# Optimization experiments

Measured on AMD Instinct MI355X. Metric: run time of the kernel, lower is better.

Reference implementation:

```python
import jax, jax.numpy as jnp
import numpy as np

B, S, D_MODEL = 2, 2048, 512
N_HEADS, D_KV = 8, 64
NUM_BUCKETS, MAX_DISTANCE = 32, 128


def _relative_position_bucket(relative_position, num_buckets=NUM_BUCKETS, max_distance=MAX_DISTANCE):
    # bidirectional (is_decoder=False) bucketing, exactly as HF T5
    num_buckets = num_buckets // 2
    buckets = (relative_position > 0).astype(jnp.int32) * num_buckets
    rel = jnp.abs(relative_position)
    max_exact = num_buckets // 2
    is_small = rel < max_exact
    rel_f = jnp.maximum(rel, 1).astype(jnp.float32)
    val_if_large = max_exact + (
        jnp.log(rel_f / max_exact) / np.log(max_distance / max_exact) * (num_buckets - max_exact)
    ).astype(jnp.int32)
    val_if_large = jnp.minimum(val_if_large, num_buckets - 1)
    return buckets + jnp.where(is_small, rel, val_if_large)


def _compute_bias(rel_bias_emb, q_len, k_len):
    ctx = jnp.arange(q_len)[:, None]          # [q,1]
    mem = jnp.arange(k_len)[None, :]          # [1,k]
    buckets = _relative_position_bucket(mem - ctx)        # [q,k] int32
    bias = rel_bias_emb[buckets]                           # [q,k,H]
    return jnp.transpose(bias, (2, 0, 1))[None]            # [1,H,q,k]


def setup_inputs() -> dict:
    key = jax.random.key(0)
    ks = jax.random.split(key, 6)
    sc = 1.0 / np.sqrt(D_MODEL)
    return {
        "hidden_states": jax.random.normal(ks[0], (B, S, D_MODEL), jnp.float32),
        "Wq": jax.random.normal(ks[1], (D_MODEL, N_HEADS * D_KV), jnp.float32) * sc,
        "Wk": jax.random.normal(ks[2], (D_MODEL, N_HEADS * D_KV), jnp.float32) * sc,
        "Wv": jax.random.normal(ks[3], (D_MODEL, N_HEADS * D_KV), jnp.float32) * sc,
        "Wo": jax.random.normal(ks[4], (N_HEADS * D_KV, D_MODEL), jnp.float32) * sc,
        "rel_bias_emb": jax.random.normal(ks[5], (NUM_BUCKETS, N_HEADS), jnp.float32),
    }


def reference(hidden_states, Wq, Wk, Wv, Wo, rel_bias_emb):
    b, s, _ = hidden_states.shape

    def proj(W):  # [b,s,D] @ [D,H*Dk] -> [b,H,s,Dk]
        return (hidden_states @ W).reshape(b, s, N_HEADS, D_KV).transpose(0, 2, 1, 3)

    q = proj(Wq)
    k = proj(Wk)
    v = proj(Wv)

    # T5 attention: NO 1/sqrt(d) scaling
    scores = jnp.einsum("bhqd,bhkd->bhqk", q, k)
    position_bias = _compute_bias(rel_bias_emb, s, s)      # [1,H,s,s]
    scores = scores + position_bias
    attn = jax.nn.softmax(scores.astype(jnp.float32), axis=-1).astype(scores.dtype)
    # dropout p=0.0 in eval mode -> identity
    out = jnp.einsum("bhqk,bhkd->bhqd", attn, v)           # [b,H,s,Dk]
    out = out.transpose(0, 2, 1, 3).reshape(b, s, N_HEADS * D_KV)
    attn_output = out @ Wo                                  # [b,s,D]
    return attn_output, position_bias
```

## Files before the change

kernel.cpp:

```cpp
#include <hip/hip_runtime.h>

typedef __attribute__((ext_vector_type(8))) short short8;
typedef __attribute__((ext_vector_type(4))) float f32x4;
typedef __attribute__((ext_vector_type(16))) float f32x16;
typedef __attribute__((ext_vector_type(4))) float float4v;
typedef __attribute__((ext_vector_type(8))) float f32x8;
typedef __attribute__((ext_vector_type(4))) unsigned short us4;
typedef __attribute__((ext_vector_type(8))) unsigned short us8v;
typedef __attribute__((ext_vector_type(4))) unsigned int uint4v;

#define DEVI __device__ __forceinline__
#define MFMA16(a,b,c) __builtin_amdgcn_mfma_f32_16x16x32_bf16((a),(b),(c),0,0,0)
#define MFMA32(a,b,c) __builtin_amdgcn_mfma_f32_32x32x16_bf16((a),(b),(c),0,0,0)

DEVI unsigned short f2bf(float x) {
    unsigned u = __builtin_bit_cast(unsigned, x);
    u += 0x7FFFu + ((u >> 16) & 1u);
    return (unsigned short)(u >> 16);
}
DEVI float bf2f(unsigned short b) {
    return __builtin_bit_cast(float, ((unsigned)b) << 16);
}
DEVI unsigned cvt_pk_bf16(float lo, float hi) {
    unsigned r;
    asm("v_cvt_pk_bf16_f32 %0, %1, %2" : "=v"(r) : "v"(lo), "v"(hi));
    return r;
}

__global__ __launch_bounds__(256) void k_prep_hidden(const float* __restrict__ hid,
                                                     unsigned short* __restrict__ hh,
                                                     unsigned short* __restrict__ hl) {
    __shared__ float tile[64][65];
    const int bid = blockIdx.x;
    const int rt = bid >> 3, ct = bid & 7;
    const int t = threadIdx.x;
    const int r = t >> 2, cc = (t & 3) << 4;
    const float* sp = hid + (long)(rt * 64 + r) * 512 + ct * 64 + cc;
    #pragma unroll
    for (int j = 0; j < 16; j += 4) {
        float4v v = *reinterpret_cast<const float4v*>(sp + j);
        tile[r][cc + j + 0] = v[0];
        tile[r][cc + j + 1] = v[1];
        tile[r][cc + j + 2] = v[2];
        tile[r][cc + j + 3] = v[3];
    }
    __syncthreads();
    #pragma unroll
    for (int s = 0; s < 2; ++s) {
        int slot = t * 2 + s;
        int lane = slot & 63, i = (slot >> 6) & 3, ktl = slot >> 8;
        int ri = i * 16 + (lane & 15);
        int kc = ktl * 32 + (lane >> 4) * 8;
        us8v hv, lv;
        #pragma unroll
        for (int j = 0; j < 8; ++j) {
            float x = tile[ri][kc + j];
            unsigned short hb = f2bf(x);
            hv[j] = hb; lv[j] = f2bf(x - bf2f(hb));
        }
        long o = ((long)(rt * 16 + ct * 2 + ktl) * 4 + i) * 512 + lane * 8;
        *reinterpret_cast<us8v*>(hh + o) = hv;
        *reinterpret_cast<us8v*>(hl + o) = lv;
    }
}

__global__ __launch_bounds__(256) void k_prep_w(const float* __restrict__ wq, const float* __restrict__ wk,
                                                const float* __restrict__ wvp, const float* __restrict__ wo,
                                                unsigned short* __restrict__ wqthi, unsigned short* __restrict__ wqtlo,
                                                unsigned short* __restrict__ wkthi, unsigned short* __restrict__ wktlo,
                                                unsigned short* __restrict__ wvt, unsigned short* __restrict__ wot) {
    __shared__ float tile[64][65];
    const int bid = blockIdx.x;
    const int mat = bid >> 6, t6 = bid & 63;
    const int tr = t6 >> 3, tc = t6 & 7;
    const float* src = mat == 0 ? wq : mat == 1 ? wk : mat == 2 ? wvp : wo;
    const int t = threadIdx.x;
    const int r = t >> 2, cc = (t & 3) << 4;
    const float* sp = src + (long)(tr * 64 + r) * 512 + tc * 64 + cc;
    #pragma unroll
    for (int j = 0; j < 16; j += 4) {
        float4v v = *reinterpret_cast<const float4v*>(sp + j);
        tile[r][cc + j + 0] = v[0];
        tile[r][cc + j + 1] = v[1];
        tile[r][cc + j + 2] = v[2];
        tile[r][cc + j + 3] = v[3];
    }
    __syncthreads();
    us8v h0, h1, l0, l1;
    #pragma unroll
    for (int j = 0; j < 8; ++j) {
        float x = tile[cc + j][r];
        unsigned short hb = f2bf(x);
        h0[j] = hb; l0[j] = f2bf(x - bf2f(hb));
        float y = tile[cc + 8 + j][r];
        unsigned short hb2 = f2bf(y);
        h1[j] = hb2; l1[j] = f2bf(y - bf2f(hb2));
    }
    if (mat <= 2) {
        const int jj = r >> 4, li = r & 15;
        const int kt = (tr * 64 + cc) >> 5;
        const int g0 = (cc >> 3) & 3;
        const long bse = ((long)((tc * 16 + kt) * 4 + jj)) * 512;
        const long o0 = bse + (g0 * 16 + li) * 8;
        const long o1 = bse + ((g0 + 1) * 16 + li) * 8;
        if (mat <= 1) {
            unsigned short* oh = mat ? wkthi : wqthi;
            unsigned short* ol = mat ? wktlo : wqtlo;
            *reinterpret_cast<us8v*>(oh + o0) = h0;
            *reinterpret_cast<us8v*>(oh + o1) = h1;
            *reinterpret_cast<us8v*>(ol + o0) = l0;
            *reinterpret_cast<us8v*>(ol + o1) = l1;
        } else {
            *reinterpret_cast<us8v*>(wvt + o0) = h0;
            *reinterpret_cast<us8v*>(wvt + o1) = h1;
        }
    } else {
        const long obase = (long)(tc * 64 + r) * 512 + tr * 64 + cc;
        *reinterpret_cast<us8v*>(wot + obase) = h0;
        *reinterpret_cast<us8v*>(wot + obase + 8) = h1;
    }
}

DEVI int bucket_large(int a) {
    if (a < 12) return 8;
    if (a < 16) return 9;
    if (a < 23) return 10;
    if (a < 32) return 11;
    if (a < 46) return 12;
    if (a < 64) return 13;
    if (a < 91) return 14;
    return 15;
}
__global__ __launch_bounds__(256) void k_prep_bias(const float* __restrict__ emb, float* __restrict__ biasT) {
    int t = blockIdx.x * 256 + threadIdx.x;
    if (t >= 8 * 4095) return;
    int h = t / 4095;
    int idx = t - h * 4095;
    int rel = idx - 2047;
    int a = rel < 0 ? -rel : rel;
    int bucket = (rel > 0 ? 16 : 0) + (a < 8 ? a : bucket_large(a));
    biasT[h * 4096 + idx] = emb[bucket * 8 + h];
}

__global__ __launch_bounds__(256) void k_proj(const unsigned short* __restrict__ hh,
                                              const unsigned short* __restrict__ hl,
                                              const unsigned short* __restrict__ wqthi, const unsigned short* __restrict__ wqtlo,
                                              const unsigned short* __restrict__ wkthi, const unsigned short* __restrict__ wktlo,
                                              const unsigned short* __restrict__ wvt,
                                              unsigned short* __restrict__ q_hi, unsigned short* __restrict__ q_lo,
                                              unsigned short* __restrict__ ktiles,
                                              unsigned short* __restrict__ vtiles) {
    const int wgid = blockIdx.x;
    const int nt = wgid % 12, mt = wgid / 12;
    const int sec = nt >> 2;
    const bool isv = (sec == 2);
    const int tid = threadIdx.x, wv = tid >> 6, lane = tid & 63;
    const int wr = wv >> 1, wc = wv & 1;
    const int g = lane >> 4, li = lane & 15;
    const int m0 = mt * 128 + wr * 64;
    const int n0 = (nt & 3) * 128 + wc * 64;
    const unsigned short* bh_ = (sec == 0) ? wqthi : (sec == 1) ? wkthi : wvt;
    const unsigned short* bl_ = (sec == 0) ? wqtlo : wktlo;
    const int rt2 = m0 >> 6;
    const int ntile = n0 >> 6;

    f32x4 zf = {0.f, 0.f, 0.f, 0.f};
    f32x4 acc[4][4];
    #pragma unroll
    for (int i = 0; i < 4; ++i)
        #pragma unroll
        for (int j = 0; j < 4; ++j) acc[i][j] = zf;

    for (int ks = 0; ks < 512; ks += 32) {
        const int kt = ks >> 5;
        const long abase = ((long)(rt2 * 16 + kt) * 4) * 512 + lane * 8;
        const long bbase = ((long)(ntile * 16 + kt) * 4) * 512 + lane * 8;
        short8 ah[4], al[4], bhf[4], blf[4];
        #pragma unroll
        for (int i = 0; i < 4; ++i) {
            ah[i] = *reinterpret_cast<const short8*>(hh + abase + i * 512);
            if (!isv) al[i] = *reinterpret_cast<const short8*>(hl + abase + i * 512);
            bhf[i] = *reinterpret_cast<const short8*>(bh_ + bbase + i * 512);
            if (!isv) blf[i] = *reinterpret_cast<const short8*>(bl_ + bbase + i * 512);
        }
        #pragma unroll
        for (int i = 0; i < 4; ++i)
            #pragma unroll
            for (int j = 0; j < 4; ++j) {
                acc[i][j] = MFMA16(ah[i], bhf[j], acc[i][j]);
                if (!isv) {
                    acc[i][j] = MFMA16(ah[i], blf[j], acc[i][j]);
                    acc[i][j] = MFMA16(al[i], bhf[j], acc[i][j]);
                }
            }
    }

    if (sec == 0) {
        #pragma unroll
        for (int i = 0; i < 4; ++i) {
            int rowb = m0 + i * 16 + g * 4;
            #pragma unroll
            for (int j = 0; j < 4; ++j) {
                int col = n0 + j * 16 + li;
                #pragma unroll
                for (int r = 0; r < 4; ++r) {
                    float x = acc[i][j][r];
                    unsigned short hb = f2bf(x);
                    long o = (long)(rowb + r) * 512 + col;
                    q_hi[o] = hb;
                    q_lo[o] = f2bf(x - bf2f(hb));
                }
            }
        }
    } else if (sec == 1) {
        #pragma unroll
        for (int i = 0; i < 4; ++i) {
            int rowb = m0 + i * 16 + g * 4;
            #pragma unroll
            for (int j = 0; j < 4; ++j) {
                int col = n0 + j * 16 + li;
                int h2 = col >> 6, d = col & 63;
                int ds2 = d >> 4, j2 = d & 7, lhalf = (d >> 3) & 1;
                #pragma unroll
                for (int r = 0; r < 4; ++r) {
                    int srow = rowb + r;
                    int bloc = srow >> 11, k = srow & 2047;
                    long base = (long)((bloc * 8 + h2) * 64 + (k >> 5)) * 4096
                              + (((k & 31) | (lhalf << 5)) * 8 + j2);
                    float x = acc[i][j][r];
                    unsigned short hb = f2bf(x);
                    ktiles[base + ds2 * 512] = hb;
                    ktiles[base + (4 + ds2) * 512] = f2bf(x - bf2f(hb));
                }
            }
        }
    } else {
        #pragma unroll
        for (int i = 0; i < 4; ++i) {
            int rowb = m0 + i * 16 + g * 4;
            int bloc = rowb >> 11, k = rowb & 2047;
            int kt = k >> 5, t = (k >> 4) & 1, lhalf = (k >> 3) & 1, j0 = k & 7;
            #pragma unroll
            for (int j = 0; j < 4; ++j) {
                int col = n0 + j * 16 + li;
                int h2 = col >> 6, d = col & 63;
                int dblk = d >> 5;
                us4 w;
                #pragma unroll
                for (int r = 0; r < 4; ++r) w[r] = f2bf(acc[i][j][r]);
                long off2 = (long)((bloc * 8 + h2) * 64 + kt) * 2048
                          + (dblk * 2 + t) * 512 + (((d & 31) | (lhalf << 5)) * 8 + j0);
                *reinterpret_cast<us4*>(vtiles + off2) = w;
            }
        }
    }
}

__global__ __launch_bounds__(128) void k_attn(const unsigned short* __restrict__ qhi,
                                              const unsigned short* __restrict__ qlo,
                                              const unsigned short* __restrict__ ktiles,
                                              const unsigned short* __restrict__ vtiles,
                                              const float* __restrict__ biasT,
                                              unsigned short* __restrict__ ctx) {
    __shared__ float lb[2080];
    __shared__ float mrg[64][34];
    const int wg = blockIdx.x;
    const int bh = wg >> 6, qt = wg & 63;
    const int b = bh >> 3, h = bh & 7;
    const int tid = threadIdx.x;
    const int kh = tid >> 6, lane = tid & 63;
    const int ql_ = lane & 31, hi = lane >> 5;
    const int q0 = qt * 32;

    for (int i = tid; i < 2080; i += 128) lb[i] = biasT[h * 4096 + (2016 - q0) + i];
    __syncthreads();

    const int q = q0 + ql_;
    const long rowQ = (long)(b * 2048 + q) * 512 + h * 64 + hi * 8;
    short8 qfh[4], qfl[4];
    #pragma unroll
    for (int ds = 0; ds < 4; ++ds) {
        qfh[ds] = *reinterpret_cast<const short8*>(qhi + rowQ + ds * 16);
        qfl[ds] = *reinterpret_cast<const short8*>(qlo + rowQ + ds * 16);
    }
    const int kbeg = kh * 1024;
    const unsigned short* ktb = ktiles + ((long)bh * 64 + (kbeg >> 5)) * 4096;
    const unsigned short* vtb = vtiles + ((long)bh * 64 + (kbeg >> 5)) * 2048;

    f32x16 o0, o1;
    #pragma unroll
    for (int i = 0; i < 16; ++i) { o0[i] = 0.f; o1[i] = 0.f; }
    float m_run = -__builtin_inff(), l_run = 0.f;

    short8 kAh[4], kAl[4], kBh[4], kBl[4], vA[4], vB[4];
    #pragma unroll
    for (int ds = 0; ds < 4; ++ds) {
        kAh[ds] = *reinterpret_cast<const short8*>(ktb + ds * 512 + lane * 8);
        kAl[ds] = *reinterpret_cast<const short8*>(ktb + (4 + ds) * 512 + lane * 8);
    }
    #pragma unroll
    for (int i = 0; i < 4; ++i)
        vA[i] = *reinterpret_cast<const short8*>(vtb + i * 512 + lane * 8);

    auto step = [&](short8 (&ckh)[4], short8 (&ckl)[4], short8 (&cv)[4],
                    short8 (&nkh)[4], short8 (&nkl)[4], short8 (&nv)[4], int it) {
        f32x16 ssA, ssB;
        #pragma unroll
        for (int i = 0; i < 16; ++i) { ssA[i] = 0.f; ssB[i] = 0.f; }
        #pragma unroll
        for (int ds = 0; ds < 4; ++ds) {
            ssA = MFMA32(ckh[ds], qfh[ds], ssA);
            ssB = MFMA32(ckh[ds], qfl[ds], ssB);
        }
        #pragma unroll
        for (int ds = 0; ds < 4; ++ds)
            ssA = MFMA32(ckl[ds], qfh[ds], ssA);
        const long ko = (it + 1 < 32) ? (long)(it + 1) * 4096 : (long)it * 4096;
        const long vo = (it + 1 < 32) ? (long)(it + 1) * 2048 : (long)it * 2048;
        #pragma unroll
        for (int ds = 0; ds < 4; ++ds) {
            nkh[ds] = *reinterpret_cast<const short8*>(ktb + ko + ds * 512 + lane * 8);
            nkl[ds] = *reinterpret_cast<const short8*>(ktb + ko + (4 + ds) * 512 + lane * 8);
        }
        #pragma unroll
        for (int i = 0; i < 4; ++i)
            nv[i] = *reinterpret_cast<const short8*>(vtb + vo + i * 512 + lane * 8);
        const int k0 = kbeg + it * 32;
        const int ib = k0 - ql_ + 31 + 4 * hi;
        float s[16];
        #pragma unroll
        for (int r = 0; r < 16; ++r)
            s[r] = (ssA[r] + ssB[r]) + lb[ib + (r & 3) + 8 * (r >> 2)];
        float t0 = fmaxf(s[0], s[1]), t1 = fmaxf(s[2], s[3]), t2 = fmaxf(s[4], s[5]), t3 = fmaxf(s[6], s[7]);
        float t4 = fmaxf(s[8], s[9]), t5 = fmaxf(s[10], s[11]), t6 = fmaxf(s[12], s[13]), t7 = fmaxf(s[14], s[15]);
        float u0 = fmaxf(t0, t1), u1 = fmaxf(t2, t3), u2 = fmaxf(t4, t5), u3 = fmaxf(t6, t7);
        float mx = fmaxf(fmaxf(u0, u1), fmaxf(u2, u3));
        mx = fmaxf(mx, __shfl_xor(mx, 32));
        bool grown = mx > m_run;
        float mnew = fmaxf(m_run, mx);
        float scale = __expf(m_run - mnew);
        float p[16];
        #pragma unroll
        for (int r = 0; r < 16; ++r) p[r] = __expf(s[r] - mnew);
        unsigned W[8];
        float ps[8];
        #pragma unroll
        for (int r2 = 0; r2 < 8; ++r2) {
            unsigned w = cvt_pk_bf16(p[2 * r2], p[2 * r2 + 1]);
            W[r2] = w;
            float plo = __builtin_bit_cast(float, w << 16);
            float phi = __builtin_bit_cast(float, w & 0xFFFF0000u);
            ps[r2] = plo + phi;
        }
        float psum = ((ps[0] + ps[1]) + (ps[2] + ps[3])) + ((ps[4] + ps[5]) + (ps[6] + ps[7]));
        l_run = l_run * scale + psum;
        m_run = mnew;
        if (__any(grown)) {
            #pragma unroll
            for (int i = 0; i < 16; ++i) { o0[i] *= scale; o1[i] *= scale; }
        }
        unsigned Sw[8];
        #pragma unroll
        for (int r2 = 0; r2 < 8; ++r2) Sw[r2] = __shfl_xor(W[r2], 32);
        #pragma unroll
        for (int t = 0; t < 2; ++t) {
            uint4v bw;
            bw[0] = hi ? Sw[4 * t + 2] : W[4 * t + 0];
            bw[1] = hi ? Sw[4 * t + 3] : W[4 * t + 1];
            bw[2] = hi ? W[4 * t + 2] : Sw[4 * t + 0];
            bw[3] = hi ? W[4 * t + 3] : Sw[4 * t + 1];
            short8 pf = __builtin_bit_cast(short8, bw);
            o0 = MFMA32(cv[t], pf, o0);
            o1 = MFMA32(cv[2 + t], pf, o1);
        }
    };

    for (int it2 = 0; it2 < 32; it2 += 2) {
        step(kAh, kAl, vA, kBh, kBl, vB, it2);
        step(kBh, kBl, vB, kAh, kAl, vA, it2 + 1);
    }

    if (kh == 1) {
        float* mp = &mrg[lane][0];
        mp[0] = m_run; mp[1] = l_run;
        #pragma unroll
        for (int i = 0; i < 16; ++i) { mp[2 + i] = o0[i]; mp[18 + i] = o1[i]; }
    }
    __syncthreads();
    if (kh == 0) {
        const float* mp = &mrg[lane][0];
        float m2 = mp[0], l2 = mp[1];
        float ms = fmaxf(m_run, m2);
        float a1 = __expf(m_run - ms);
        float a2 = __expf(m2 - ms);
        float lt = l_run * a1 + l2 * a2;
        lt += __shfl_xor(lt, 32);
        float inv = 1.0f / lt;
        const long crow = (long)(b * 2048 + q) * 512 + h * 64;
        #pragma unroll
        for (int a = 0; a < 4; ++a) {
            us4 w0, w1;
            #pragma unroll
            for (int c = 0; c < 4; ++c) {
                w0[c] = f2bf((o0[4 * a + c] * a1 + mp[2 + 4 * a + c] * a2) * inv);
                w1[c] = f2bf((o1[4 * a + c] * a1 + mp[18 + 4 * a + c] * a2) * inv);
            }
            *reinterpret_cast<us4*>(ctx + crow + 8 * a + 4 * hi) = w0;
            *reinterpret_cast<us4*>(ctx + crow + 32 + 8 * a + 4 * hi) = w1;
        }
    }
}

__global__ __launch_bounds__(256) void k_oproj(const unsigned short* __restrict__ ctx,
                                               const unsigned short* __restrict__ wot,
                                               float* __restrict__ outp) {
    const int wgid = blockIdx.x;
    const int nt = wgid & 3, mt = wgid >> 2;
    const int tid = threadIdx.x, wv = tid >> 6, lane = tid & 63;
    const int wr = wv >> 1, wc = wv & 1;
    const int g = lane >> 4, li = lane & 15;
    const int m0 = mt * 128 + wr * 64;
    const int n0 = nt * 128 + wc * 64;

    f32x4 zf = {0.f, 0.f, 0.f, 0.f};
    f32x4 acc[4][4];
    #pragma unroll
    for (int i = 0; i < 4; ++i)
        #pragma unroll
        for (int j = 0; j < 4; ++j) acc[i][j] = zf;

    for (int ks = 0; ks < 512; ks += 32) {
        int koff = ks + g * 8;
        short8 af[4], bf[4];
        #pragma unroll
        for (int i = 0; i < 4; ++i) {
            af[i] = *reinterpret_cast<const short8*>(ctx + (long)(m0 + i * 16 + li) * 512 + koff);
            bf[i] = *reinterpret_cast<const short8*>(wot + (long)(n0 + i * 16 + li) * 512 + koff);
        }
        #pragma unroll
        for (int i = 0; i < 4; ++i)
            #pragma unroll
            for (int j = 0; j < 4; ++j)
                acc[i][j] = MFMA16(af[i], bf[j], acc[i][j]);
    }
    #pragma unroll
    for (int i = 0; i < 4; ++i) {
        int rowb = m0 + i * 16 + g * 4;
        #pragma unroll
        for (int j = 0; j < 4; ++j) {
            int col = n0 + j * 16 + li;
            #pragma unroll
            for (int r = 0; r < 4; ++r)
                outp[(long)(rowb + r) * 512 + col] = acc[i][j][r];
        }
    }
}

__global__ __launch_bounds__(256) void k_biasout(const float* __restrict__ biasT,
                                                 float* __restrict__ outb) {
    long t = (long)blockIdx.x * 256 + threadIdx.x;
    int h = (int)(t >> 19);
    long r = t & 524287;
    int qq = (int)(r >> 8);
    int k8 = (int)(r & 255) * 8;
    const float* src = biasT + h * 4096 + (k8 - qq + 2047);
    f32x8 w;
    #pragma unroll
    for (int i = 0; i < 8; ++i) w[i] = src[i];
    *reinterpret_cast<f32x8*>(outb + t * 8) = w;
}

extern "C" void kernel_launch(void* const* d_in, const int* in_sizes, int n_in,
                              void* d_out, int out_size, void* d_ws, size_t ws_size,
                              hipStream_t stream) {
    const float* hidden = (const float*)d_in[0];
    const float* Wq = (const float*)d_in[1];
    const float* Wk = (const float*)d_in[2];
    const float* Wv = (const float*)d_in[3];
    const float* Wo = (const float*)d_in[4];
    const float* emb = (const float*)d_in[5];
    float* out = (float*)d_out;

    char* ws = (char*)d_ws;
    size_t off = 0;
    auto alloc = [&](size_t bytes) { char* p = ws + off; off += (bytes + 255) & ~(size_t)255; return p; };

    unsigned short* hid_hi = (unsigned short*)alloc(4096ull * 512 * 2);
    unsigned short* hid_lo = (unsigned short*)alloc(4096ull * 512 * 2);
    unsigned short* wqthi  = (unsigned short*)alloc(512ull * 512 * 2);
    unsigned short* wqtlo  = (unsigned short*)alloc(512ull * 512 * 2);
    unsigned short* wkthi  = (unsigned short*)alloc(512ull * 512 * 2);
    unsigned short* wktlo  = (unsigned short*)alloc(512ull * 512 * 2);
    unsigned short* wvt    = (unsigned short*)alloc(512ull * 512 * 2);
    unsigned short* wot    = (unsigned short*)alloc(512ull * 512 * 2);
    float*          biasT  = (float*)alloc(8ull * 4096 * 4);
    unsigned short* q_hi   = (unsigned short*)alloc(4096ull * 512 * 2);
    unsigned short* q_lo   = (unsigned short*)alloc(4096ull * 512 * 2);
    unsigned short* ktiles = (unsigned short*)alloc(16ull * 64 * 8 * 512 * 2);
    unsigned short* vtiles = (unsigned short*)alloc(16ull * 64 * 4 * 512 * 2);
    unsigned short* ctx    = (unsigned short*)alloc(4096ull * 512 * 2);

    k_prep_hidden<<<512, 256, 0, stream>>>(hidden, hid_hi, hid_lo);
    k_prep_w<<<256, 256, 0, stream>>>(Wq, Wk, Wv, Wo, wqthi, wqtlo, wkthi, wktlo, wvt, wot);
    k_prep_bias<<<128, 256, 0, stream>>>(emb, biasT);
    k_proj<<<384, 256, 0, stream>>>(hid_hi, hid_lo, wqthi, wqtlo, wkthi, wktlo, wvt,
                                    q_hi, q_lo, ktiles, vtiles);
    k_attn<<<1024, 128, 0, stream>>>(q_hi, q_lo, ktiles, vtiles, biasT, ctx);
    k_oproj<<<128, 256, 0, stream>>>(ctx, wot, out);
    k_biasout<<<16384, 256, 0, stream>>>(biasT, out + 2097152);
}
```

Measured before the change: 143.8 us.

## Store ctx and Wo in MFMA fragment-packed layout and raise MFMA priority

The attention kernel now writes its bf16 context output directly in a tiled fragment layout, and the Wo transpose uses the same packed layout as the Q/K/V weights. The output projection can then load each operand fragment with contiguous per-lane 16-byte reads instead of strided row loads. It also wraps the MFMA blocks in the attention loop with s_setprio to favor matrix issue over other waves. Producer and consumer indexing must agree exactly, and the priority hints may have little or no effect.

Result: faster. 139.2 us (-3.2%).

```diff
diff --git a/kernel.cpp b/kernel.cpp
--- a/kernel.cpp
+++ b/kernel.cpp
@@ -96,28 +96,23 @@
         unsigned short hb2 = f2bf(y);
         h1[j] = hb2; l1[j] = f2bf(y - bf2f(hb2));
     }
-    if (mat <= 2) {
-        const int jj = r >> 4, li = r & 15;
-        const int kt = (tr * 64 + cc) >> 5;
-        const int g0 = (cc >> 3) & 3;
-        const long bse = ((long)((tc * 16 + kt) * 4 + jj)) * 512;
-        const long o0 = bse + (g0 * 16 + li) * 8;
-        const long o1 = bse + ((g0 + 1) * 16 + li) * 8;
-        if (mat <= 1) {
-            unsigned short* oh = mat ? wkthi : wqthi;
-            unsigned short* ol = mat ? wktlo : wqtlo;
-            *reinterpret_cast<us8v*>(oh + o0) = h0;
-            *reinterpret_cast<us8v*>(oh + o1) = h1;
-            *reinterpret_cast<us8v*>(ol + o0) = l0;
-            *reinterpret_cast<us8v*>(ol + o1) = l1;
-        } else {
-            *reinterpret_cast<us8v*>(wvt + o0) = h0;
-            *reinterpret_cast<us8v*>(wvt + o1) = h1;
-        }
+    const int jj = r >> 4, li = r & 15;
+    const int kt = (tr * 64 + cc) >> 5;
+    const int g0 = (cc >> 3) & 3;
+    const long bse = ((long)((tc * 16 + kt) * 4 + jj)) * 512;
+    const long o0 = bse + (g0 * 16 + li) * 8;
+    const long o1 = bse + ((g0 + 1) * 16 + li) * 8;
+    if (mat <= 1) {
+        unsigned short* oh = mat ? wkthi : wqthi;
+        unsigned short* ol = mat ? wktlo : wqtlo;
+        *reinterpret_cast<us8v*>(oh + o0) = h0;
+        *reinterpret_cast<us8v*>(oh + o1) = h1;
+        *reinterpret_cast<us8v*>(ol + o0) = l0;
+        *reinterpret_cast<us8v*>(ol + o1) = l1;
     } else {
-        const long obase = (long)(tc * 64 + r) * 512 + tr * 64 + cc;
-        *reinterpret_cast<us8v*>(wot + obase) = h0;
-        *reinterpret_cast<us8v*>(wot + obase + 8) = h1;
+        unsigned short* oh = mat == 2 ? wvt : wot;
+        *reinterpret_cast<us8v*>(oh + o0) = h0;
+        *reinterpret_cast<us8v*>(oh + o1) = h1;
     }
 }
 
@@ -307,6 +302,7 @@
         f32x16 ssA, ssB;
         #pragma unroll
         for (int i = 0; i < 16; ++i) { ssA[i] = 0.f; ssB[i] = 0.f; }
+        __builtin_amdgcn_s_setprio(1);
         #pragma unroll
         for (int ds = 0; ds < 4; ++ds) {
             ssA = MFMA32(ckh[ds], qfh[ds], ssA);
@@ -315,6 +311,7 @@
         #pragma unroll
         for (int ds = 0; ds < 4; ++ds)
             ssA = MFMA32(ckl[ds], qfh[ds], ssA);
+        __builtin_amdgcn_s_setprio(0);
         const long ko = (it + 1 < 32) ? (long)(it + 1) * 4096 : (long)it * 4096;
         const long vo = (it + 1 < 32) ? (long)(it + 1) * 2048 : (long)it * 2048;
         #pragma unroll
@@ -362,6 +359,7 @@
         unsigned Sw[8];
         #pragma unroll
         for (int r2 = 0; r2 < 8; ++r2) Sw[r2] = __shfl_xor(W[r2], 32);
+        __builtin_amdgcn_s_setprio(1);
         #pragma unroll
         for (int t = 0; t < 2; ++t) {
             uint4v bw;
@@ -373,6 +371,7 @@
             o0 = MFMA32(cv[t], pf, o0);
             o1 = MFMA32(cv[2 + t], pf, o1);
         }
+        __builtin_amdgcn_s_setprio(0);
     };
 
     for (int it2 = 0; it2 < 32; it2 += 2) {
@@ -396,7 +395,8 @@
         float lt = l_run * a1 + l2 * a2;
         lt += __shfl_xor(lt, 32);
         float inv = 1.0f / lt;
-        const long crow = (long)(b * 2048 + q) * 512 + h * 64;
+        const int rt = b * 32 + (q >> 6), ii = (q >> 4) & 3, li2 = q & 15;
+        const long baseA = ((long)(rt * 16 + 2 * h) * 4 + ii) * 512 + li2 * 8 + 4 * hi;
         #pragma unroll
         for (int a = 0; a < 4; ++a) {
             us4 w0, w1;
@@ -405,8 +405,8 @@
                 w0[c] = f2bf((o0[4 * a + c] * a1 + mp[2 + 4 * a + c] * a2) * inv);
                 w1[c] = f2bf((o1[4 * a + c] * a1 + mp[18 + 4 * a + c] * a2) * inv);
             }
-            *reinterpret_cast<us4*>(ctx + crow + 8 * a + 4 * hi) = w0;
-            *reinterpret_cast<us4*>(ctx + crow + 32 + 8 * a + 4 * hi) = w1;
+            *reinterpret_cast<us4*>(ctx + baseA + a * 128) = w0;
+            *reinterpret_cast<us4*>(ctx + baseA + 2048 + a * 128) = w1;
         }
     }
 }
@@ -421,6 +421,7 @@
     const int g = lane >> 4, li = lane & 15;
     const int m0 = mt * 128 + wr * 64;
     const int n0 = nt * 128 + wc * 64;
+    const int rt2 = m0 >> 6, ntile = n0 >> 6;
 
     f32x4 zf = {0.f, 0.f, 0.f, 0.f};
     f32x4 acc[4][4];
@@ -430,12 +431,14 @@
         for (int j = 0; j < 4; ++j) acc[i][j] = zf;
 
     for (int ks = 0; ks < 512; ks += 32) {
-        int koff = ks + g * 8;
+        const int kt = ks >> 5;
+        const long abase = (long)(rt2 * 16 + kt) * 2048 + lane * 8;
+        const long bbase = (long)(ntile * 16 + kt) * 2048 + lane * 8;
         short8 af[4], bf[4];
         #pragma unroll
         for (int i = 0; i < 4; ++i) {
-            af[i] = *reinterpret_cast<const short8*>(ctx + (long)(m0 + i * 16 + li) * 512 + koff);
-            bf[i] = *reinterpret_cast<const short8*>(wot + (long)(n0 + i * 16 + li) * 512 + koff);
+            af[i] = *reinterpret_cast<const short8*>(ctx + abase + i * 512);
+            bf[i] = *reinterpret_cast<const short8*>(wot + bbase + i * 512);
         }
         #pragma unroll
         for (int i = 0; i < 4; ++i)
```
